# Optimization experiments

Hardware: AMD Instinct MI355X
Metric: run time of the kernel (lower is better)

Reference implementation:

```python
import jax, jax.numpy as jnp
import numpy as np

N = 1_000_000   # total nodes
B = 20_000      # number of graphs (segments)
V = 100_000     # item vocab (rows of feat table)
D = 128         # input_dim
H = 128         # hidden_dim
O = 256         # output_dim
EPS = 1e-5


def setup_inputs() -> dict:
    key = jax.random.key(0)
    ks = jax.random.split(key, 10)
    feat = jax.random.normal(ks[0], (V, D), dtype=jnp.float32)
    iid = jax.random.randint(ks[1], (N,), 0, V)
    segment_ids = jnp.sort(jax.random.randint(ks[2], (N,), 0, B))
    last_nodes = jax.random.randint(ks[3], (B,), 0, N)
    s = 1.0 / np.sqrt(D)
    gamma = jnp.ones((D,), jnp.float32)
    beta = jnp.zeros((D,), jnp.float32)
    W_u = jax.random.uniform(ks[4], (D, H), jnp.float32, -s, s)
    W_v = jax.random.uniform(ks[5], (D, H), jnp.float32, -s, s)
    b_v = jax.random.uniform(ks[6], (H,), jnp.float32, -s, s)
    w_e = jax.random.uniform(ks[7], (H,), jnp.float32, -1.0 / np.sqrt(H), 1.0 / np.sqrt(H))
    W_out = jax.random.uniform(ks[8], (D, O), jnp.float32, -s, s)
    return {"feat": feat, "iid": iid, "segment_ids": segment_ids,
            "last_nodes": last_nodes, "gamma": gamma, "beta": beta,
            "W_u": W_u, "W_v": W_v, "b_v": b_v, "w_e": w_e, "W_out": W_out}


def reference(feat, iid, segment_ids, last_nodes, gamma, beta, W_u, W_v, b_v, w_e, W_out):
    # gather per-node features from item table
    x = feat[iid]                                  # [N, D]
    # BatchNorm1d (training mode: batch statistics, biased var)
    mean = jnp.mean(x, axis=0)
    var = jnp.mean((x - mean) ** 2, axis=0)
    x = (x - mean) * jax.lax.rsqrt(var + EPS) * gamma + beta
    # projections
    feat_u = x @ W_u                               # [N, H]
    feat_v = x[last_nodes] @ W_v + b_v             # [B, H]
    e = jax.nn.sigmoid(feat_u + feat_v[segment_ids]) @ w_e   # [N]
    # segment softmax over per-graph node segments
    e_max = jax.ops.segment_max(e, segment_ids, num_segments=B)
    ex = jnp.exp(e - e_max[segment_ids])
    denom = jax.ops.segment_sum(ex, segment_ids, num_segments=B)
    alpha = ex / denom[segment_ids]                # [N]
    # weighted segment sum, then output projection
    rst = jax.ops.segment_sum(x * alpha[:, None], segment_ids, num_segments=B)  # [B, D]
    return rst @ W_out                             # [B, O]
```

## Files before the change

kernel.cpp:

```cpp
#include <hip/hip_runtime.h>

typedef __attribute__((ext_vector_type(8))) short short8;
typedef __attribute__((ext_vector_type(4))) float floatx4;
typedef __attribute__((ext_vector_type(4))) int intx4;

static __device__ __forceinline__ unsigned short f2bf(float x) {
    unsigned int u = __float_as_uint(x);
    u += 0x7fffu + ((u >> 16) & 1u);
    return (unsigned short)(u >> 16);
}

template <int CTRL>
static __device__ __forceinline__ float dpp_add(float x) {
    int v = __builtin_amdgcn_update_dpp(0, __float_as_int(x), CTRL, 0xf, 0xf, true);
    return x + __int_as_float(v);
}

__global__ void k_hist(const int* __restrict__ iid, int* __restrict__ counts, int N) {
    int n = blockIdx.x * blockDim.x + threadIdx.x;
    if (n < N) atomicAdd(&counts[iid[n]], 1);
}

__global__ __launch_bounds__(256) void k_cvtstats(const float* __restrict__ feat,
                                                  const int* __restrict__ counts,
                                                  unsigned short* __restrict__ featb,
                                                  float* __restrict__ dsum, float* __restrict__ dsumsq,
                                                  int V) {
    int tid = threadIdx.x;
    int r2 = tid >> 7, d = tid & 127;
    float s = 0.f, qa = 0.f;
    for (int vp = blockIdx.x; vp * 2 < V; vp += gridDim.x) {
        int v = vp * 2 + r2;
        if (v >= V) continue;
        float f = feat[(size_t)v * 128 + d];
        featb[(size_t)v * 128 + d] = f2bf(f);
        float c = (float)counts[v];
        if (c != 0.f) { s += c * f; qa += c * f * f; }
    }
    __shared__ float red[256];
    red[tid] = s; __syncthreads();
    if (tid < 128) atomicAdd(&dsum[d], red[tid] + red[tid + 128]);
    __syncthreads();
    red[tid] = qa; __syncthreads();
    if (tid < 128) atomicAdd(&dsumsq[d], red[tid] + red[tid + 128]);
}

__global__ __launch_bounds__(128) void k_affine(const float* __restrict__ sum,
                                                const float* __restrict__ sumsq,
                                                const float* __restrict__ gamma,
                                                const float* __restrict__ beta,
                                                float* __restrict__ scale, float* __restrict__ shift,
                                                float invN) {
    int d = threadIdx.x;
    float mean = sum[d] * invN;
    float var  = sumsq[d] * invN - mean * mean;
    float sc   = gamma[d] * rsqrtf(var + 1e-5f);
    scale[d] = sc;
    shift[d] = beta[d] - mean * sc;
}

__global__ __launch_bounds__(128) void k_prep(const float* __restrict__ Wu, const float* __restrict__ Wv,
                                              const float* __restrict__ bv,
                                              const float* __restrict__ scale, const float* __restrict__ shift,
                                              unsigned short* __restrict__ wut, float* __restrict__ wvs,
                                              float* __restrict__ cbias) {
    int h = blockIdx.x, d = threadIdx.x;
    float sc = scale[d], sh = shift[d];
    float wu = Wu[d * 128 + h], wv = Wv[d * 128 + h];
    wut[h * 128 + d] = f2bf(sc * wu);
    wvs[d * 128 + h] = sc * wv;
    __shared__ float red[128];
    red[d] = sh * (wu + wv);
    __syncthreads();
    for (int off = 64; off > 0; off >>= 1) {
        if (d < off) red[d] += red[d + off];
        __syncthreads();
    }
    if (d == 0) cbias[h] = bv[h] + red[0];
}

__global__ __launch_bounds__(128) void k_fv(const float* __restrict__ feat, const int* __restrict__ iid,
                                            const int* __restrict__ last, const float* __restrict__ wvs,
                                            const float* __restrict__ cbias, float* __restrict__ fv,
                                            int B) {
    const int GPB = 8;
    int b0 = blockIdx.x * GPB;
    int h = threadIdx.x;
    __shared__ float sx[GPB][128];
    for (int g = 0; g < GPB; ++g) {
        int b = b0 + g;
        if (b < B) {
            int row = iid[last[b]];
            sx[g][h] = feat[(size_t)row * 128 + h];
        }
    }
    __syncthreads();
    float acc[GPB];
#pragma unroll
    for (int g = 0; g < GPB; ++g) acc[g] = 0.f;
    for (int d = 0; d < 128; ++d) {
        float w = wvs[d * 128 + h];
#pragma unroll
        for (int g = 0; g < GPB; ++g) acc[g] += sx[g][d] * w;
    }
    float c = cbias[h];
    for (int g = 0; g < GPB; ++g)
        if (b0 + g < B) fv[(size_t)(b0 + g) * 128 + h] = acc[g] + c;
}

__global__ __launch_bounds__(512, 4) void k_main(
        const unsigned short* __restrict__ featb, const int* __restrict__ iid,
        const int* __restrict__ seg, const unsigned short* __restrict__ wut,
        const float* __restrict__ fv, const float* __restrict__ we_g,
        float* __restrict__ rstAcc, float* __restrict__ den,
        int N, int B, int numTiles) {
    __shared__ unsigned short sA[2][64 * 128];
    __shared__ int   sSeg[2][64];
    __shared__ float sFv[2][4][128];
    __shared__ float sEp[4][64];

    const float NL2E = -1.44269504f;

    int tid = threadIdx.x;
    int wv = tid >> 6, lane = tid & 63, q = lane >> 4, c = lane & 15;
    int p2 = lane & 15;
    int wvH = wv & 3, wvM = wv >> 2;

    short8 bfr[2][4];
    float we2[2];
#pragma unroll
    for (int t = 0; t < 2; ++t) {
        int h = (2 * wvH + t) * 16 + c;
        we2[t] = we_g[h];
#pragma unroll
        for (int kc = 0; kc < 4; ++kc)
            bfr[t][kc] = *(const short8*)(wut + h * 128 + kc * 32 + q * 8);
    }

    if (blockIdx.x >= numTiles) return;

    int iidR[2]; int segR; float fvR;
    auto loadRegs = [&](int T) {
        int n0 = T << 6;
#pragma unroll
        for (int k = 0; k < 2; ++k)
            iidR[k] = iid[min(n0 + wv * 8 + 4 * k + (lane >> 4), N - 1)];
        segR = seg[min(n0 + (tid & 63), N - 1)];
        int s0 = __builtin_amdgcn_readfirstlane(segR);
        int fvrow = min(s0 + (tid >> 7), B - 1);
        fvR = NL2E * fv[(size_t)fvrow * 128 + (tid & 127)];
    };
    auto stage = [&](int buf) {
        unsigned short* sAb = &sA[buf][0];
#pragma unroll
        for (int k = 0; k < 2; ++k) {
            int row = wv * 8 + 4 * k + (lane >> 4);
            int j = (p2 & 8) | ((p2 & 7) ^ (row & 7));
            const unsigned short* g = featb + (size_t)iidR[k] * 128 + j * 8;
            __builtin_amdgcn_global_load_lds(
                (const __attribute__((address_space(1))) void*)g,
                (__attribute__((address_space(3))) void*)(sAb + wv * 1024 + k * 512),
                16, 0, 0);
        }
        if (tid < 64) sSeg[buf][tid] = segR;
        sFv[buf][tid >> 7][tid & 127] = fvR;
    };

    int T = blockIdx.x;
    loadRegs(T);
    stage(0);
    int cur = 0;

    for (;;) {
        int Tn = T + gridDim.x;
        bool hn = (Tn < numTiles);
        if (hn) loadRegs(Tn);
        __syncthreads();
        if (hn) stage(cur ^ 1);

        floatx4 acc[2][2];
#pragma unroll
        for (int mt = 0; mt < 2; ++mt)
#pragma unroll
            for (int t = 0; t < 2; ++t) acc[mt][t] = (floatx4)(0.f);
#pragma unroll
        for (int kc = 0; kc < 4; ++kc) {
            int jj = 4 * kc + q;
            int pofs = ((jj & 8) | ((jj & 7) ^ (c & 7))) * 8;
            int rb = wvM * 32;
            short8 a0 = *(const short8*)&sA[cur][(rb + 0  + c) * 128 + pofs];
            short8 a1 = *(const short8*)&sA[cur][(rb + 16 + c) * 128 + pofs];
#pragma unroll
            for (int t = 0; t < 2; ++t) {
                acc[0][t] = __builtin_amdgcn_mfma_f32_16x16x32_bf16(a0, bfr[t][kc], acc[0][t], 0, 0, 0);
                acc[1][t] = __builtin_amdgcn_mfma_f32_16x16x32_bf16(a1, bfr[t][kc], acc[1][t], 0, 0, 0);
            }
        }
        {
            int s0b = sSeg[cur][0];
            int h0 = wvH * 32 + c;
#pragma unroll
            for (int mt = 0; mt < 2; ++mt)
#pragma unroll
                for (int r = 0; r < 4; ++r) {
                    int nl = wvM * 32 + mt * 16 + q * 4 + r;
                    int sg = sSeg[cur][nl];
                    int off = sg - s0b;
                    float f0, f1;
                    if (off < 4) {
                        f0 = sFv[cur][off][h0];
                        f1 = sFv[cur][off][h0 + 16];
                    } else {
                        f0 = NL2E * fv[((size_t)sg << 7) + h0];
                        f1 = NL2E * fv[((size_t)sg << 7) + h0 + 16];
                    }
                    float m0 = __builtin_fmaf(acc[mt][0][r], NL2E, f0);
                    float m1 = __builtin_fmaf(acc[mt][1][r], NL2E, f1);
                    float p = we2[0] * __builtin_amdgcn_rcpf(1.f + __builtin_amdgcn_exp2f(m0))
                            + we2[1] * __builtin_amdgcn_rcpf(1.f + __builtin_amdgcn_exp2f(m1));
                    p = dpp_add<0xb1>(p);
                    p = dpp_add<0x4e>(p);
                    p = dpp_add<0x141>(p);
                    p = dpp_add<0x140>(p);
                    if (c == 0) sEp[wvH][nl] = p;
                }
        }
        __syncthreads();

        if (wv < 4) {
            int n0t = T << 6;
            int nb = wv * 16;
            int d0 = lane * 2;
            int jj = lane >> 2;
            int wsub = (lane & 3) * 4;
            const char* base = (const char*)&sA[cur][0];
            float a0 = 0.f, a1 = 0.f, dl = 0.f;
            int curseg = sSeg[cur][nb];
#pragma unroll
            for (int jh = 0; jh < 2; ++jh) {
                float exr[8];
                int sgr[8];
#pragma unroll
                for (int jg = 0; jg < 2; ++jg) {
                    int rb = nb + jh * 8 + jg * 4;
                    floatx4 e0 = *(const floatx4*)&sEp[0][rb];
                    floatx4 e1 = *(const floatx4*)&sEp[1][rb];
                    floatx4 e2 = *(const floatx4*)&sEp[2][rb];
                    floatx4 e3 = *(const floatx4*)&sEp[3][rb];
                    *(intx4*)&sgr[jg * 4] = *(const intx4*)&sSeg[cur][rb];
#pragma unroll
                    for (int r = 0; r < 4; ++r) {
                        float s = e0[r] + e1[r] + e2[r] + e3[r];
                        exr[jg * 4 + r] = (n0t + rb + r < N) ? __expf(s) : 0.f;
                    }
                }
#pragma unroll
                for (int j = 0; j < 8; ++j) {
                    int row = nb + jh * 8 + j;
                    int sg = sgr[j];
                    if (sg != curseg) {
                        atomicAdd(&rstAcc[(size_t)curseg * 128 + d0], a0);
                        atomicAdd(&rstAcc[(size_t)curseg * 128 + d0 + 1], a1);
                        if (lane == 0) atomicAdd(&den[curseg], dl);
                        a0 = a1 = dl = 0.f; curseg = sg;
                    }
                    int ch = (jj & 8) | ((jj & 7) ^ (row & 7));
                    unsigned u = *(const unsigned*)(base + row * 256 + ch * 16 + wsub);
                    float e = exr[j];
                    a0 += e * __uint_as_float(u << 16);
                    a1 += e * __uint_as_float(u & 0xffff0000u);
                    dl += e;
                }
            }
            atomicAdd(&rstAcc[(size_t)curseg * 128 + d0], a0);
            atomicAdd(&rstAcc[(size_t)curseg * 128 + d0 + 1], a1);
            if (lane == 0) atomicAdd(&den[curseg], dl);
        }

        if (!hn) break;
        T = Tn; cur ^= 1;
    }
}

__global__ __launch_bounds__(256) void k_out(const float* __restrict__ rstAcc,
                                             const float* __restrict__ den,
                                             const float* __restrict__ scale,
                                             const float* __restrict__ shift,
                                             const float* __restrict__ Wout,
                                             float* __restrict__ out, int B) {
    __shared__ float sT[128][36];
    __shared__ float sInv[32];
    int b0 = blockIdx.x * 32;
    int t = threadIdx.x;
    for (int i = 0; i < 16; ++i) {
        int idx = i * 256 + t;
        int r = idx >> 7, d = idx & 127;
        int b = min(b0 + r, B - 1);
        sT[d][r] = scale[d] * rstAcc[((size_t)b << 7) + d];
    }
    if (t < 32) {
        int b = min(b0 + t, B - 1);
        float dn = den[b];
        sInv[t] = (dn > 0.f) ? 1.f / dn : 0.f;
    }
    __syncthreads();
    float acc[32];
#pragma unroll
    for (int r = 0; r < 32; ++r) acc[r] = 0.f;
    float sb = 0.f;
    for (int dd = 0; dd < 128; ++dd) {
        float w = Wout[dd * 256 + t];
        sb += shift[dd] * w;
        const float4* row = (const float4*)&sT[dd][0];
#pragma unroll
        for (int r4 = 0; r4 < 8; ++r4) {
            float4 v = row[r4];
            acc[r4 * 4 + 0] += w * v.x;
            acc[r4 * 4 + 1] += w * v.y;
            acc[r4 * 4 + 2] += w * v.z;
            acc[r4 * 4 + 3] += w * v.w;
        }
    }
    for (int r = 0; r < 32; ++r)
        if (b0 + r < B) {
            float inv = sInv[r];
            out[(size_t)(b0 + r) * 256 + t] = acc[r] * inv + (inv != 0.f ? sb : 0.f);
        }
}

extern "C" void kernel_launch(void* const* d_in, const int* in_sizes, int n_in,
                              void* d_out, int out_size, void* d_ws, size_t ws_size,
                              hipStream_t stream) {
    const float* feat  = (const float*)d_in[0];
    const int*   iid   = (const int*)d_in[1];
    const int*   seg   = (const int*)d_in[2];
    const int*   last  = (const int*)d_in[3];
    const float* gamma = (const float*)d_in[4];
    const float* beta  = (const float*)d_in[5];
    const float* Wu    = (const float*)d_in[6];
    const float* Wv    = (const float*)d_in[7];
    const float* bv    = (const float*)d_in[8];
    const float* we    = (const float*)d_in[9];
    const float* Wout  = (const float*)d_in[10];
    float* out = (float*)d_out;

    int V = in_sizes[0] / 128;
    int N = in_sizes[1];
    int B = in_sizes[3];

    char* w = (char*)d_ws;
    size_t off = 0;
    auto alloc = [&](size_t bytes) -> void* {
        void* p = w + off;
        off += (bytes + 255) & ~(size_t)255;
        return p;
    };
    int*   counts = (int*)alloc((size_t)V * 4);
    float* dsum   = (float*)alloc(512);
    float* dsumsq = (float*)alloc(512);
    float* rstAcc = (float*)alloc((size_t)B * 128 * 4);
    float* den    = (float*)alloc((size_t)B * 4);
    size_t zero_bytes = off;
    float* scale  = (float*)alloc(512);
    float* shift  = (float*)alloc(512);
    float* cbias  = (float*)alloc(512);
    unsigned short* wut = (unsigned short*)alloc(128 * 128 * 2);
    float* wvs    = (float*)alloc(128 * 128 * 4);
    float* fv     = (float*)alloc((size_t)B * 128 * 4);
    unsigned short* featb = (unsigned short*)alloc((size_t)V * 128 * 2);
    (void)ws_size; (void)n_in; (void)out_size;

    hipMemsetAsync(d_ws, 0, zero_bytes, stream);

    k_hist<<<(N + 255) / 256, 256, 0, stream>>>(iid, counts, N);
    k_cvtstats<<<1024, 256, 0, stream>>>(feat, counts, featb, dsum, dsumsq, V);
    k_affine<<<1, 128, 0, stream>>>(dsum, dsumsq, gamma, beta, scale, shift, 1.0f / (float)N);
    k_prep<<<128, 128, 0, stream>>>(Wu, Wv, bv, scale, shift, wut, wvs, cbias);
    k_fv<<<(B + 7) / 8, 128, 0, stream>>>(feat, iid, last, wvs, cbias, fv, B);

    int numTiles = (N + 63) / 64;
    k_main<<<1024, 512, 0, stream>>>(featb, iid, seg, wut, fv, we, rstAcc, den, N, B, numTiles);

    k_out<<<(B + 31) / 32, 256, 0, stream>>>(rstAcc, den, scale, shift, Wout, out, B);
}
```

Baseline: 427.4 us.

## Shrink k_main tiles to 32 nodes with 256-thread blocks and all-wave aggregation

The main kernel now processes 32-node tiles with 4 waves per block instead of 64-node tiles with 8 waves. Each wave covers a 32-column slice of the hidden dimension for all 32 rows, and all four waves share the weighted segment-sum phase instead of only half the waves doing it. The launch uses more blocks (1792) with a higher occupancy target, so the old idle half-block phase disappears and latency hiding should improve. In exchange the per-tile barrier and staging overhead doubles relative to work, and more atomics are flushed at tile boundaries.

```diff
diff --git a/kernel.cpp b/kernel.cpp
--- a/kernel.cpp
+++ b/kernel.cpp
@@ -108,29 +108,28 @@
         if (b0 + g < B) fv[(size_t)(b0 + g) * 128 + h] = acc[g] + c;
 }
 
-__global__ __launch_bounds__(512, 4) void k_main(
+__global__ __launch_bounds__(256, 6) void k_main(
         const unsigned short* __restrict__ featb, const int* __restrict__ iid,
         const int* __restrict__ seg, const unsigned short* __restrict__ wut,
         const float* __restrict__ fv, const float* __restrict__ we_g,
         float* __restrict__ rstAcc, float* __restrict__ den,
         int N, int B, int numTiles) {
-    __shared__ unsigned short sA[2][64 * 128];
-    __shared__ int   sSeg[2][64];
+    __shared__ unsigned short sA[2][32 * 128];
+    __shared__ int   sSeg[2][32];
     __shared__ float sFv[2][4][128];
-    __shared__ float sEp[4][64];
+    __shared__ float sEp[4][32];
 
     const float NL2E = -1.44269504f;
 
     int tid = threadIdx.x;
     int wv = tid >> 6, lane = tid & 63, q = lane >> 4, c = lane & 15;
     int p2 = lane & 15;
-    int wvH = wv & 3, wvM = wv >> 2;
 
     short8 bfr[2][4];
     float we2[2];
 #pragma unroll
     for (int t = 0; t < 2; ++t) {
-        int h = (2 * wvH + t) * 16 + c;
+        int h = (2 * wv + t) * 16 + c;
         we2[t] = we_g[h];
 #pragma unroll
         for (int kc = 0; kc < 4; ++kc)
@@ -139,31 +138,34 @@
 
     if (blockIdx.x >= numTiles) return;
 
-    int iidR[2]; int segR; float fvR;
+    int iidR[2]; int segR; float2 fvR;
     auto loadRegs = [&](int T) {
-        int n0 = T << 6;
-#pragma unroll
-        for (int k = 0; k < 2; ++k)
-            iidR[k] = iid[min(n0 + wv * 8 + 4 * k + (lane >> 4), N - 1)];
-        segR = seg[min(n0 + (tid & 63), N - 1)];
+        int n0 = T << 5;
+#pragma unroll
+        for (int k = 0; k < 2; ++k) {
+            int row = k * 16 + wv * 4 + (lane >> 4);
+            iidR[k] = iid[min(n0 + row, N - 1)];
+        }
+        segR = seg[min(n0 + (tid & 31), N - 1)];
         int s0 = __builtin_amdgcn_readfirstlane(segR);
-        int fvrow = min(s0 + (tid >> 7), B - 1);
-        fvR = NL2E * fv[(size_t)fvrow * 128 + (tid & 127)];
+        int fvrow = min(s0 + (tid >> 6), B - 1);
+        fvR = *(const float2*)(fv + (size_t)fvrow * 128 + ((tid << 1) & 127));
+        fvR.x *= NL2E; fvR.y *= NL2E;
     };
     auto stage = [&](int buf) {
         unsigned short* sAb = &sA[buf][0];
 #pragma unroll
         for (int k = 0; k < 2; ++k) {
-            int row = wv * 8 + 4 * k + (lane >> 4);
+            int row = k * 16 + wv * 4 + (lane >> 4);
             int j = (p2 & 8) | ((p2 & 7) ^ (row & 7));
             const unsigned short* g = featb + (size_t)iidR[k] * 128 + j * 8;
             __builtin_amdgcn_global_load_lds(
                 (const __attribute__((address_space(1))) void*)g,
-                (__attribute__((address_space(3))) void*)(sAb + wv * 1024 + k * 512),
+                (__attribute__((address_space(3))) void*)(sAb + k * 2048 + wv * 512),
                 16, 0, 0);
         }
-        if (tid < 64) sSeg[buf][tid] = segR;
-        sFv[buf][tid >> 7][tid & 127] = fvR;
+        if (tid < 32) sSeg[buf][tid] = segR;
+        *(float2*)&sFv[buf][tid >> 6][(tid << 1) & 127] = fvR;
     };
 
     int T = blockIdx.x;
@@ -187,9 +189,8 @@
         for (int kc = 0; kc < 4; ++kc) {
             int jj = 4 * kc + q;
             int pofs = ((jj & 8) | ((jj & 7) ^ (c & 7))) * 8;
-            int rb = wvM * 32;
-            short8 a0 = *(const short8*)&sA[cur][(rb + 0  + c) * 128 + pofs];
-            short8 a1 = *(const short8*)&sA[cur][(rb + 16 + c) * 128 + pofs];
+            short8 a0 = *(const short8*)&sA[cur][( 0 + c) * 128 + pofs];
+            short8 a1 = *(const short8*)&sA[cur][(16 + c) * 128 + pofs];
 #pragma unroll
             for (int t = 0; t < 2; ++t) {
                 acc[0][t] = __builtin_amdgcn_mfma_f32_16x16x32_bf16(a0, bfr[t][kc], acc[0][t], 0, 0, 0);
@@ -198,12 +199,12 @@
         }
         {
             int s0b = sSeg[cur][0];
-            int h0 = wvH * 32 + c;
+            int h0 = wv * 32 + c;
 #pragma unroll
             for (int mt = 0; mt < 2; ++mt)
 #pragma unroll
                 for (int r = 0; r < 4; ++r) {
-                    int nl = wvM * 32 + mt * 16 + q * 4 + r;
+                    int nl = mt * 16 + q * 4 + r;
                     int sg = sSeg[cur][nl];
                     int off = sg - s0b;
                     float f0, f1;
@@ -222,55 +223,52 @@
                     p = dpp_add<0x4e>(p);
                     p = dpp_add<0x141>(p);
                     p = dpp_add<0x140>(p);
-                    if (c == 0) sEp[wvH][nl] = p;
+                    if (c == 0) sEp[wv][nl] = p;
                 }
         }
         __syncthreads();
 
-        if (wv < 4) {
-            int n0t = T << 6;
-            int nb = wv * 16;
+        {
+            int n0t = T << 5;
+            int nb = wv * 8;
+            float exr[8];
+            int sgr[8];
+#pragma unroll
+            for (int jg = 0; jg < 2; ++jg) {
+                int rb = nb + jg * 4;
+                floatx4 e0 = *(const floatx4*)&sEp[0][rb];
+                floatx4 e1 = *(const floatx4*)&sEp[1][rb];
+                floatx4 e2 = *(const floatx4*)&sEp[2][rb];
+                floatx4 e3 = *(const floatx4*)&sEp[3][rb];
+                *(intx4*)&sgr[jg * 4] = *(const intx4*)&sSeg[cur][rb];
+#pragma unroll
+                for (int r = 0; r < 4; ++r) {
+                    float s = e0[r] + e1[r] + e2[r] + e3[r];
+                    exr[jg * 4 + r] = (n0t + rb + r < N) ? __expf(s) : 0.f;
+                }
+            }
             int d0 = lane * 2;
             int jj = lane >> 2;
             int wsub = (lane & 3) * 4;
             const char* base = (const char*)&sA[cur][0];
             float a0 = 0.f, a1 = 0.f, dl = 0.f;
-            int curseg = sSeg[cur][nb];
-#pragma unroll
-            for (int jh = 0; jh < 2; ++jh) {
-                float exr[8];
-                int sgr[8];
-#pragma unroll
-                for (int jg = 0; jg < 2; ++jg) {
-                    int rb = nb + jh * 8 + jg * 4;
-                    floatx4 e0 = *(const floatx4*)&sEp[0][rb];
-                    floatx4 e1 = *(const floatx4*)&sEp[1][rb];
-                    floatx4 e2 = *(const floatx4*)&sEp[2][rb];
-                    floatx4 e3 = *(const floatx4*)&sEp[3][rb];
-                    *(intx4*)&sgr[jg * 4] = *(const intx4*)&sSeg[cur][rb];
-#pragma unroll
-                    for (int r = 0; r < 4; ++r) {
-                        float s = e0[r] + e1[r] + e2[r] + e3[r];
-                        exr[jg * 4 + r] = (n0t + rb + r < N) ? __expf(s) : 0.f;
-                    }
+            int curseg = sgr[0];
+#pragma unroll
+            for (int j = 0; j < 8; ++j) {
+                int row = nb + j;
+                int sg = sgr[j];
+                if (sg != curseg) {
+                    atomicAdd(&rstAcc[(size_t)curseg * 128 + d0], a0);
+                    atomicAdd(&rstAcc[(size_t)curseg * 128 + d0 + 1], a1);
+                    if (lane == 0) atomicAdd(&den[curseg], dl);
+                    a0 = a1 = dl = 0.f; curseg = sg;
                 }
-#pragma unroll
-                for (int j = 0; j < 8; ++j) {
-                    int row = nb + jh * 8 + j;
-                    int sg = sgr[j];
-                    if (sg != curseg) {
-                        atomicAdd(&rstAcc[(size_t)curseg * 128 + d0], a0);
-                        atomicAdd(&rstAcc[(size_t)curseg * 128 + d0 + 1], a1);
-                        if (lane == 0) atomicAdd(&den[curseg], dl);
-                        a0 = a1 = dl = 0.f; curseg = sg;
-                    }
-                    int ch = (jj & 8) | ((jj & 7) ^ (row & 7));
-                    unsigned u = *(const unsigned*)(base + row * 256 + ch * 16 + wsub);
-                    float e = exr[j];
-                    a0 += e * __uint_as_float(u << 16);
-                    a1 += e * __uint_as_float(u & 0xffff0000u);
-                    dl += e;
-                }
+                int ch = (jj & 8) | ((jj & 7) ^ (row & 7));
+                unsigned u = *(const unsigned*)(base + row * 256 + ch * 16 + wsub);
+                float e = exr[j];
+                a0 += e * __uint_as_float(u << 16);
+                a1 += e * __uint_as_float(u & 0xffff0000u);
+                dl += e;
             }
             atomicAdd(&rstAcc[(size_t)curseg * 128 + d0], a0);
             atomicAdd(&rstAcc[(size_t)curseg * 128 + d0 + 1], a1);
@@ -378,8 +376,8 @@
     k_prep<<<128, 128, 0, stream>>>(Wu, Wv, bv, scale, shift, wut, wvs, cbias);
     k_fv<<<(B + 7) / 8, 128, 0, stream>>>(feat, iid, last, wvs, cbias, fv, B);
 
-    int numTiles = (N + 63) / 64;
-    k_main<<<1024, 512, 0, stream>>>(featb, iid, seg, wut, fv, we, rstAcc, den, N, B, numTiles);
+    int numTiles = (N + 31) / 32;
+    k_main<<<1792, 256, 0, stream>>>(featb, iid, seg, wut, fv, we, rstAcc, den, N, B, numTiles);
 
     k_out<<<(B + 31) / 32, 256, 0, stream>>>(rstAcc, den, scale, shift, Wout, out, B);
 }
```

Result: slower. 573.0 us (+34.1%).
